# Performance work log

Measured on AMD Instinct MI355X. Metric: run time of the kernel, lower is better.

## Reference

```python
import jax, jax.numpy as jnp
import numpy as np

Qn, Y, X = 9, 2048, 2048
VUY, PR, ALPHA1, ALPHA01, MUY = 1.4, 0.71, 1.35, 1.05, 0.01
UAX, UAY = 0.0, 0.0
EX_INT = [1, 0, -1, 0, 1, -1, -1, 1, 0]
EY_INT = [0, 1, 0, -1, 1, 1, -1, -1, 0]
EX = jnp.asarray(EX_INT, jnp.float32) + UAX
EY = jnp.asarray(EY_INT, jnp.float32) + UAY
ICV = VUY - 1.0   # 1/Cv
CV = 1.0 / ICV
# streaming shifts: Y_indices = (y - (-ey1)) % Y, X_indices = (x - ex1) % X
# gathering with those indices == jnp.roll(field, (-ey1, ex1))
SHIFTS = [(-EY_INT[q], EX_INT[q]) for q in range(Qn)]


def setup_inputs() -> dict:
    key = jax.random.key(0)
    k1, k2, k3 = jax.random.split(key, 3)
    F = jax.random.uniform(k1, (Qn, Y, X), jnp.float32)
    G = jax.random.uniform(k2, (Qn, Y, X), jnp.float32)
    Feq = jax.random.uniform(k3, (Qn, Y, X), jnp.float32)
    return {"F": F, "G": G, "Feq": Feq}


def reference(F, G, Feq):
    # ---- macroscopic moments ----
    rho = jnp.clip(jnp.sum(F, axis=0), 1e-6)              # (Y, X)
    inv_rho = 1.0 / rho
    ux = jnp.einsum('q,qyx->yx', EX, F) * inv_rho
    uy = jnp.einsum('q,qyx->yx', EY, F) * inv_rho
    E = jnp.sum(G, axis=0) * 0.5 * inv_rho
    # ---- temperature from energy ----
    uu = ux * ux + uy * uy
    T = jnp.clip(ICV * (E - uu * 0.5), 1e-6)
    # ---- Maxwellian heat flux ----
    rhoH2 = 2.0 * rho * (E + T)
    qx = rhoH2 * ux
    qy = rhoH2 * uy
    # ---- G-weights ----
    one_minus_T = 1.0 - T
    w = jnp.concatenate([
        jnp.broadcast_to((one_minus_T * T * 0.5)[None], (4, Y, X)),
        jnp.broadcast_to((T * T * 0.25)[None], (4, Y, X)),
        (one_minus_T * one_minus_T)[None],
    ], axis=0)                                             # (Qn, Y, X)
    # ---- adaptive relaxation times ----
    tau_DL = MUY / (rho * T) + 0.5
    EPS = jnp.mean(jnp.abs(F - Feq) / (Feq + 1e-10), axis=0)
    alpha = jnp.ones_like(EPS)
    alpha = jnp.where(EPS < 0.01, 1.0, alpha)
    alpha = jnp.where(EPS < 0.1, ALPHA01, alpha)
    alpha = jnp.where(EPS < 1.0, ALPHA1, alpha)
    alpha = jnp.where(EPS >= 1.0, jax.lax.stop_gradient(1.0 / tau_DL), alpha)  # .detach()
    tau = alpha * tau_DL
    tauT = 0.5 + (tau - 0.5) / PR
    omega = 1.0 / tau
    omegaT = 1.0 / tauT
    # ---- BGK collision on F + periodic-shift streaming ----
    F_post = F - omega[None] * (F - Feq)
    F_str = jnp.stack([jnp.roll(F_post[q], SHIFTS[q], axis=(0, 1)) for q in range(Qn)], axis=0)
    # pack all moment outputs with the streamed field: (Qn + Qn + 8, Y, X)
    fields = jnp.stack([rho, ux, uy, E, T, qx, qy, omegaT], axis=0)
    return jnp.concatenate([F_str, w, fields], axis=0)
```

## Files before the change

### kernel.cpp

```cpp
#include <hip/hip_runtime.h>

namespace {

constexpr int QN = 9;
constexpr int YD = 2048;
constexpr int XD = 2048;

constexpr float PRc     = 0.71f;
constexpr float ALPHA1c = 1.35f;
constexpr float MUYc    = 0.01f;
constexpr float ICVc    = 1.4f - 1.0f;

typedef float fvec2 __attribute__((ext_vector_type(2)));

__device__ __forceinline__ float rcpf(float x) { return __builtin_amdgcn_rcpf(x); }

__global__ __launch_bounds__(256) void lb_fused(
    const float* __restrict__ Fin,
    const float* __restrict__ Gin,
    const float* __restrict__ Feqin,
    float* __restrict__ out)
{
    constexpr int EXI[QN] = {1, 0, -1, 0, 1, -1, -1, 1, 0};
    constexpr int EYI[QN] = {0, 1, 0, -1, 1, 1, -1, -1, 0};

    const int tid  = blockIdx.x * 256 + threadIdx.x;
    const int lane = threadIdx.x & 63;
    const int x0   = (tid & (XD / 2 - 1)) * 2;
    const int y    = tid >> 10;
    const size_t plane = (size_t)YD * XD;
    const size_t base  = (size_t)y * XD + x0;

    float f[QN][2];
    float feq[QN][2];
    float sumG[2] = {0.f, 0.f};

    #pragma unroll
    for (int q = 0; q < QN; ++q) {
        const fvec2 fv = __builtin_nontemporal_load(
            reinterpret_cast<const fvec2*>(Fin   + q * plane + base));
        const fvec2 fe = __builtin_nontemporal_load(
            reinterpret_cast<const fvec2*>(Feqin + q * plane + base));
        const fvec2 gv = __builtin_nontemporal_load(
            reinterpret_cast<const fvec2*>(Gin   + q * plane + base));
        f[q][0] = fv.x;   f[q][1] = fv.y;
        feq[q][0] = fe.x; feq[q][1] = fe.y;
        sumG[0] += gv.x;  sumG[1] += gv.y;
    }

    float rho[2], ux[2], uy[2], E[2], T[2], qx[2], qy[2], omgT[2], omg[2];
    float wA[2], wB[2], wC[2];

    #pragma unroll
    for (int j = 0; j < 2; ++j) {
        float s = 0.f;
        #pragma unroll
        for (int q = 0; q < QN; ++q) s += f[q][j];
        const float r  = fmaxf(s, 1e-6f);
        const float ir = rcpf(r);
        const float vx = (f[0][j] - f[2][j] + f[4][j] - f[5][j] - f[6][j] + f[7][j]) * ir;
        const float vy = (f[1][j] - f[3][j] + f[4][j] + f[5][j] - f[6][j] - f[7][j]) * ir;
        const float e  = sumG[j] * 0.5f * ir;
        const float uu = vx * vx + vy * vy;
        const float t  = fmaxf(ICVc * (e - 0.5f * uu), 1e-6f);
        const float rhoH2 = 2.0f * r * (e + t);
        const float one_mt = 1.0f - t;

        float eps = 0.f;
        #pragma unroll
        for (int q = 0; q < QN; ++q)
            eps += fabsf(f[q][j] - feq[q][j]) * rcpf(feq[q][j] + 1e-10f);
        eps *= (1.0f / 9.0f);

        const float tau_DL = MUYc * rcpf(r * t) + 0.5f;
        const float alpha  = (eps < 1.0f) ? ALPHA1c : rcpf(tau_DL);
        const float tau    = alpha * tau_DL;
        const float tauT   = 0.5f + (tau - 0.5f) * (1.0f / PRc);

        omg[j]  = rcpf(tau);
        omgT[j] = rcpf(tauT);
        rho[j] = r; ux[j] = vx; uy[j] = vy; E[j] = e; T[j] = t;
        qx[j] = rhoH2 * vx; qy[j] = rhoH2 * vy;
        wA[j] = one_mt * t * 0.5f;
        wB[j] = t * t * 0.25f;
        wC[j] = one_mt * one_mt;
    }

    const size_t row0 = (size_t)y * XD;
    const size_t rowm = (size_t)((y - 1) & (YD - 1)) * XD;
    const size_t rowp = (size_t)((y + 1) & (YD - 1)) * XD;

    #pragma unroll
    for (int q = 0; q < QN; ++q) {
        const int ey = EYI[q];
        const size_t rowb = (ey == 0) ? row0 : ((ey == 1) ? rowm : rowp);
        const float fp0 = f[q][0] - omg[0] * (f[q][0] - feq[q][0]);
        const float fp1 = f[q][1] - omg[1] * (f[q][1] - feq[q][1]);
        float* oplane = out + q * plane + rowb;
        const int ex = EXI[q];
        if (ex == 0) {
            fvec2 pv; pv.x = fp0; pv.y = fp1;
            __builtin_nontemporal_store(pv, reinterpret_cast<fvec2*>(oplane + x0));
        } else {
            const float nb = __shfl_down(fp0, 1);
            fvec2 pv; pv.x = fp1; pv.y = nb;
            const int xp = (ex == 1) ? (x0 + 2) : x0;
            if (lane != 63)
                __builtin_nontemporal_store(pv, reinterpret_cast<fvec2*>(oplane + xp));
            if (lane == 0)
                oplane[(x0 + ex) & (XD - 1)] = fp0;
            if (lane == 63)
                oplane[(x0 + 1 + ex) & (XD - 1)] = fp1;
        }
    }

    auto store2 = [&](int p, const float* v) {
        fvec2 pv; pv.x = v[0]; pv.y = v[1];
        __builtin_nontemporal_store(pv,
            reinterpret_cast<fvec2*>(out + (size_t)p * plane + base));
    };
    store2(9, wA);  store2(10, wA); store2(11, wA); store2(12, wA);
    store2(13, wB); store2(14, wB); store2(15, wB); store2(16, wB);
    store2(17, wC);
    store2(18, rho); store2(19, ux); store2(20, uy); store2(21, E);
    store2(22, T);   store2(23, qx); store2(24, qy); store2(25, omgT);
}

}

extern "C" void kernel_launch(void* const* d_in, const int* in_sizes, int n_in,
                              void* d_out, int out_size, void* d_ws, size_t ws_size,
                              hipStream_t stream) {
    const float* F   = (const float*)d_in[0];
    const float* G   = (const float*)d_in[1];
    const float* Feq = (const float*)d_in[2];
    float* out = (float*)d_out;

    const int total_threads = (XD / 2) * YD;
    const int block = 256;
    const int grid  = total_threads / block;
    lb_fused<<<grid, block, 0, stream>>>(F, G, Feq, out);
}
```

Baseline: 187.6 us.

## Process one cell per thread with scalar loads and direct shifted stores

Switches from two cells per thread with float2 vector accesses to one cell per thread with scalar loads and stores. The streaming step no longer uses a cross-lane shuffle with boundary-lane fixups; each thread writes its post-collision value directly to the wrapped shifted address, even when that address is misaligned. The moment and weight stores are moved ahead of the streaming stores. This doubles thread count and lowers register pressure per thread, at the cost of narrower memory transactions.

```diff
diff --git a/kernel.cpp b/kernel.cpp
--- a/kernel.cpp
+++ b/kernel.cpp
@@ -11,8 +11,6 @@
 constexpr float MUYc    = 0.01f;
 constexpr float ICVc    = 1.4f - 1.0f;
 
-typedef float fvec2 __attribute__((ext_vector_type(2)));
-
 __device__ __forceinline__ float rcpf(float x) { return __builtin_amdgcn_rcpf(x); }
 
 __global__ __launch_bounds__(256) void lb_fused(
@@ -24,67 +22,62 @@
     constexpr int EXI[QN] = {1, 0, -1, 0, 1, -1, -1, 1, 0};
     constexpr int EYI[QN] = {0, 1, 0, -1, 1, 1, -1, -1, 0};
 
-    const int tid  = blockIdx.x * 256 + threadIdx.x;
-    const int lane = threadIdx.x & 63;
-    const int x0   = (tid & (XD / 2 - 1)) * 2;
-    const int y    = tid >> 10;
+    const int tid = blockIdx.x * 256 + threadIdx.x;
+    const int x   = tid & (XD - 1);
+    const int y   = tid >> 11;
     const size_t plane = (size_t)YD * XD;
-    const size_t base  = (size_t)y * XD + x0;
+    const size_t base  = (size_t)y * XD + x;
 
-    float f[QN][2];
-    float feq[QN][2];
-    float sumG[2] = {0.f, 0.f};
+    float f[QN];
+    float feq[QN];
+    float sumG = 0.f;
 
     #pragma unroll
     for (int q = 0; q < QN; ++q) {
-        const fvec2 fv = __builtin_nontemporal_load(
-            reinterpret_cast<const fvec2*>(Fin   + q * plane + base));
-        const fvec2 fe = __builtin_nontemporal_load(
-            reinterpret_cast<const fvec2*>(Feqin + q * plane + base));
-        const fvec2 gv = __builtin_nontemporal_load(
-            reinterpret_cast<const fvec2*>(Gin   + q * plane + base));
-        f[q][0] = fv.x;   f[q][1] = fv.y;
-        feq[q][0] = fe.x; feq[q][1] = fe.y;
-        sumG[0] += gv.x;  sumG[1] += gv.y;
+        f[q]   = __builtin_nontemporal_load(Fin   + q * plane + base);
+        feq[q] = __builtin_nontemporal_load(Feqin + q * plane + base);
+        sumG  += __builtin_nontemporal_load(Gin   + q * plane + base);
     }
 
-    float rho[2], ux[2], uy[2], E[2], T[2], qx[2], qy[2], omgT[2], omg[2];
-    float wA[2], wB[2], wC[2];
+    float s = 0.f;
+    #pragma unroll
+    for (int q = 0; q < QN; ++q) s += f[q];
+    const float r  = fmaxf(s, 1e-6f);
+    const float ir = rcpf(r);
+    const float vx = (f[0] - f[2] + f[4] - f[5] - f[6] + f[7]) * ir;
+    const float vy = (f[1] - f[3] + f[4] + f[5] - f[6] - f[7]) * ir;
+    const float e  = sumG * 0.5f * ir;
+    const float uu = vx * vx + vy * vy;
+    const float t  = fmaxf(ICVc * (e - 0.5f * uu), 1e-6f);
+    const float rhoH2 = 2.0f * r * (e + t);
+    const float one_mt = 1.0f - t;
 
+    float eps = 0.f;
     #pragma unroll
-    for (int j = 0; j < 2; ++j) {
-        float s = 0.f;
-        #pragma unroll
-        for (int q = 0; q < QN; ++q) s += f[q][j];
-        const float r  = fmaxf(s, 1e-6f);
-        const float ir = rcpf(r);
-        const float vx = (f[0][j] - f[2][j] + f[4][j] - f[5][j] - f[6][j] + f[7][j]) * ir;
-        const float vy = (f[1][j] - f[3][j] + f[4][j] + f[5][j] - f[6][j] - f[7][j]) * ir;
-        const float e  = sumG[j] * 0.5f * ir;
-        const float uu = vx * vx + vy * vy;
-        const float t  = fmaxf(ICVc * (e - 0.5f * uu), 1e-6f);
-        const float rhoH2 = 2.0f * r * (e + t);
-        const float one_mt = 1.0f - t;
+    for (int q = 0; q < QN; ++q)
+        eps += fabsf(f[q] - feq[q]) * rcpf(feq[q] + 1e-10f);
+    eps *= (1.0f / 9.0f);
 
-        float eps = 0.f;
-        #pragma unroll
-        for (int q = 0; q < QN; ++q)
-            eps += fabsf(f[q][j] - feq[q][j]) * rcpf(feq[q][j] + 1e-10f);
-        eps *= (1.0f / 9.0f);
+    const float tau_DL = MUYc * rcpf(r * t) + 0.5f;
+    const float alpha  = (eps < 1.0f) ? ALPHA1c : rcpf(tau_DL);
+    const float tau    = alpha * tau_DL;
+    const float tauT   = 0.5f + (tau - 0.5f) * (1.0f / PRc);
+    const float omg    = rcpf(tau);
+    const float omgT   = rcpf(tauT);
 
-        const float tau_DL = MUYc * rcpf(r * t) + 0.5f;
-        const float alpha  = (eps < 1.0f) ? ALPHA1c : rcpf(tau_DL);
-        const float tau    = alpha * tau_DL;
-        const float tauT   = 0.5f + (tau - 0.5f) * (1.0f / PRc);
+    const float wA = one_mt * t * 0.5f;
+    const float wB = t * t * 0.25f;
+    const float wC = one_mt * one_mt;
 
-        omg[j]  = rcpf(tau);
-        omgT[j] = rcpf(tauT);
-        rho[j] = r; ux[j] = vx; uy[j] = vy; E[j] = e; T[j] = t;
-        qx[j] = rhoH2 * vx; qy[j] = rhoH2 * vy;
-        wA[j] = one_mt * t * 0.5f;
-        wB[j] = t * t * 0.25f;
-        wC[j] = one_mt * one_mt;
-    }
+    auto store1 = [&](int p, float v) {
+        __builtin_nontemporal_store(v, out + (size_t)p * plane + base);
+    };
+    store1(9, wA);  store1(10, wA); store1(11, wA); store1(12, wA);
+    store1(13, wB); store1(14, wB); store1(15, wB); store1(16, wB);
+    store1(17, wC);
+    store1(18, r);    store1(19, vx);          store1(20, vy);
+    store1(21, e);    store1(22, t);           store1(23, rhoH2 * vx);
+    store1(24, rhoH2 * vy); store1(25, omgT);
 
     const size_t row0 = (size_t)y * XD;
     const size_t rowm = (size_t)((y - 1) & (YD - 1)) * XD;
@@ -94,36 +87,10 @@
     for (int q = 0; q < QN; ++q) {
         const int ey = EYI[q];
         const size_t rowb = (ey == 0) ? row0 : ((ey == 1) ? rowm : rowp);
-        const float fp0 = f[q][0] - omg[0] * (f[q][0] - feq[q][0]);
-        const float fp1 = f[q][1] - omg[1] * (f[q][1] - feq[q][1]);
-        float* oplane = out + q * plane + rowb;
-        const int ex = EXI[q];
-        if (ex == 0) {
-            fvec2 pv; pv.x = fp0; pv.y = fp1;
-            __builtin_nontemporal_store(pv, reinterpret_cast<fvec2*>(oplane + x0));
-        } else {
-            const float nb = __shfl_down(fp0, 1);
-            fvec2 pv; pv.x = fp1; pv.y = nb;
-            const int xp = (ex == 1) ? (x0 + 2) : x0;
-            if (lane != 63)
-                __builtin_nontemporal_store(pv, reinterpret_cast<fvec2*>(oplane + xp));
-            if (lane == 0)
-                oplane[(x0 + ex) & (XD - 1)] = fp0;
-            if (lane == 63)
-                oplane[(x0 + 1 + ex) & (XD - 1)] = fp1;
-        }
+        const float fp = f[q] - omg * (f[q] - feq[q]);
+        const int xp = (x + EXI[q]) & (XD - 1);
+        __builtin_nontemporal_store(fp, out + q * plane + rowb + xp);
     }
-
-    auto store2 = [&](int p, const float* v) {
-        fvec2 pv; pv.x = v[0]; pv.y = v[1];
-        __builtin_nontemporal_store(pv,
-            reinterpret_cast<fvec2*>(out + (size_t)p * plane + base));
-    };
-    store2(9, wA);  store2(10, wA); store2(11, wA); store2(12, wA);
-    store2(13, wB); store2(14, wB); store2(15, wB); store2(16, wB);
-    store2(17, wC);
-    store2(18, rho); store2(19, ux); store2(20, uy); store2(21, E);
-    store2(22, T);   store2(23, qx); store2(24, qy); store2(25, omgT);
 }
 
 }
@@ -136,7 +103,7 @@
     const float* Feq = (const float*)d_in[2];
     float* out = (float*)d_out;
 
-    const int total_threads = (XD / 2) * YD;
+    const int total_threads = XD * YD;
     const int block = 256;
     const int grid  = total_threads / block;
     lb_fused<<<grid, block, 0, stream>>>(F, G, Feq, out);
```

Result: slower. 206.3 us (+9.9%).
